# Kernel optimization log

Hardware: AMD Instinct MI355X
Metric: run time of the kernel (lower is better)

The kernel has to match this reference:

```python
import jax, jax.numpy as jnp
import numpy as np

N = 40000      # nodes
D = 64         # nnodefeatures
DEG = 32       # avg in-degree
E = N * DEG    # edges
G = 200        # graphs in batch
ATT = 64       # attention_size
HID = 128      # cls_hidden_dim
NCLS = 6
NLAYERS = 3


def setup_inputs() -> dict:
    key = jax.random.key(0)
    ks = jax.random.split(key, 8)
    s = 0.05
    x = jax.random.normal(ks[0], (N, D), dtype=jnp.float32)
    row = jax.random.randint(ks[1], (E,), 0, N, dtype=jnp.int32)
    # every node appears as a target exactly DEG times -> no zero degrees
    col = jnp.repeat(jnp.arange(N, dtype=jnp.int32), DEG)
    edge_index = jnp.stack([row, col])
    batch = jnp.repeat(jnp.arange(G, dtype=jnp.int32), N // G)
    W_lin = jax.random.normal(ks[2], (D, D), jnp.float32) * s
    b_lin = jnp.zeros((D,), jnp.float32)
    W_att = jax.random.normal(ks[3], (ATT, 2 * D), jnp.float32) * s
    a_vec = jnp.ones((ATT, 1), jnp.float32)  # torch.ones init
    W1 = jax.random.normal(ks[4], (HID, D), jnp.float32) * s
    b1 = jnp.zeros((HID,), jnp.float32)
    W2 = jax.random.normal(ks[5], (NCLS, HID), jnp.float32) * s
    b2 = jnp.zeros((NCLS,), jnp.float32)
    return dict(x=x, W_lin=W_lin, b_lin=b_lin, W_att=W_att, a_vec=a_vec,
                W1=W1, b1=b1, W2=W2, b2=b2,
                edge_index=edge_index, batch=batch, n_graphs=G)


def _gnn_layer(x, row, col, W_lin, b_lin, W_att, a_vec):
    n = x.shape[0]
    deg = jnp.sqrt(jax.ops.segment_sum(jnp.ones_like(col, dtype=x.dtype), col, num_segments=n))
    deg = jnp.where(jnp.isinf(deg), jnp.zeros_like(deg), deg)  # deg[deg==inf]=0
    norm = deg[row] * deg[col]                                  # [E]
    x_j = x[row]                                                # [E, D] gather source
    x_i = x[col]                                                # [E, D] gather target
    att_in = jnp.concatenate([x_j, x_i], axis=-1)               # [E, 2D]
    score = jnp.exp((att_in @ W_att.T) @ a_vec)                 # [E, 1]
    att_norm = jax.ops.segment_sum(score, col, num_segments=n)  # [N, 1] (scatter by edge_index[1])
    att = score / att_norm[row]                                 # gathered at edge_index[0] (faithful)
    m = ((x_j * att) @ W_lin.T + b_lin) / norm[:, None]         # [E, D]
    out = jax.ops.segment_sum(m, col, num_segments=n)           # aggregate by target
    return jax.nn.selu(out)


def reference(x, W_lin, b_lin, W_att, a_vec, W1, b1, W2, b2, edge_index, batch, n_graphs):
    row, col = edge_index[0], edge_index[1]
    # Faithful to original: the loop re-applies the layer to the ORIGINAL x each time
    for _ in range(NLAYERS):
        h = _gnn_layer(x, row, col, W_lin, b_lin, W_att, a_vec)
    sums = jax.ops.segment_sum(h, batch, num_segments=n_graphs)
    counts = jax.ops.segment_sum(jnp.ones((x.shape[0],), x.dtype), batch, num_segments=n_graphs)
    pooled = sums / counts[:, None]                              # global_mean_pool
    hcls = jax.nn.selu(pooled @ W1.T + b1)
    logits = hcls @ W2.T + b2
    return jax.nn.softmax(logits, axis=-1)
```

## Files before the change

kernel.cpp:

```cpp
#include <hip/hip_runtime.h>
#include <hip/hip_bf16.h>
#include <stdint.h>

#define N_NODES 40000
#define D_FEAT 64
#define DEG 32
#define E_EDGES (N_NODES * DEG)
#define G_GRAPHS 200
#define NPG 200
#define ATT_SZ 64
#define HID 128
#define NCLS 6
#define XS 69

__device__ __forceinline__ float selu_f(float x) {
    const float scale = 1.0507009873554805f;
    const float alpha = 1.6732632423543772f;
    return scale * (x > 0.f ? x : alpha * (__expf(x) - 1.f));
}

__device__ __forceinline__ uint32_t f2bf(float f) {
    uint32_t u = __builtin_bit_cast(uint32_t, f);
    return (u + 0x7fffu + ((u >> 16) & 1u)) >> 16;
}
__device__ __forceinline__ float bflo(uint32_t u) { return __builtin_bit_cast(float, u << 16); }
__device__ __forceinline__ float bfhi(uint32_t u) { return __builtin_bit_cast(float, u & 0xffff0000u); }

__global__ __launch_bounds__(256) void k_node(const float* __restrict__ x,
                                              const float* __restrict__ Wlin,
                                              const float* __restrict__ Watt,
                                              const float* __restrict__ avec,
                                              float* __restrict__ P,
                                              float* __restrict__ Q,
                                              uint32_t* __restrict__ yb,
                                              float* __restrict__ pool) {
    __shared__ float xs[160 * XS];
    __shared__ float ws[64 * XS];
    __shared__ float ws_w[128];
    int tid = threadIdx.x;
    int n0 = blockIdx.x * 160;
    if (blockIdx.x < 50) pool[blockIdx.x * 256 + tid] = 0.f;

    const float4* x4 = (const float4*)(x + (size_t)n0 * 64);
    const float4* W4 = (const float4*)Wlin;
#pragma unroll
    for (int s = 0; s < 10; ++s) {
        int idx = tid + s * 256, r = idx >> 4, kk = idx & 15;
        *(float4*)&xs[r * XS + kk * 4] = x4[idx];
    }
#pragma unroll
    for (int s = 0; s < 4; ++s) {
        int idx = tid + s * 256, r = idx >> 4, kk = idx & 15;
        *(float4*)&ws[r * XS + kk * 4] = W4[idx];
    }
    if (tid < 128) {
        float s = 0.f;
        for (int k = 0; k < ATT_SZ; ++k) s += avec[k] * Watt[k * 128 + tid];
        ws_w[tid] = s;
    }
    __syncthreads();

    if (tid < 160) {
        float s1 = 0.f, s2 = 0.f;
#pragma unroll 8
        for (int k = 0; k < 64; ++k) {
            float xv = xs[tid * XS + k];
            s1 += xv * ws_w[k];
            s2 += xv * ws_w[64 + k];
        }
        P[n0 + tid] = __expf(s1);
        Q[n0 + tid] = __expf(s2);
    }

    int tm = tid >> 4, tf = tid & 15;
    float acc[10][4];
#pragma unroll
    for (int i = 0; i < 10; ++i)
#pragma unroll
        for (int j = 0; j < 4; ++j) acc[i][j] = 0.f;
#pragma unroll
    for (int kk = 0; kk < 16; ++kk) {
        float4 wv[4];
#pragma unroll
        for (int j = 0; j < 4; ++j) wv[j] = *(const float4*)&ws[(4 * tf + j) * XS + kk * 4];
#pragma unroll
        for (int i = 0; i < 10; ++i) {
            float4 xv = *(const float4*)&xs[(tm + 16 * i) * XS + kk * 4];
#pragma unroll
            for (int j = 0; j < 4; ++j)
                acc[i][j] += xv.x * wv[j].x + xv.y * wv[j].y
                           + xv.z * wv[j].z + xv.w * wv[j].w;
        }
    }
#pragma unroll
    for (int i = 0; i < 10; ++i) {
        int m = n0 + tm + 16 * i;
        uint32_t p0 = f2bf(acc[i][0]) | (f2bf(acc[i][1]) << 16);
        uint32_t p1 = f2bf(acc[i][2]) | (f2bf(acc[i][3]) << 16);
        *(uint2*)&yb[(size_t)m * 32 + tf * 2] = make_uint2(p0, p1);
    }
}

__global__ __launch_bounds__(256) void k_edges(const int* __restrict__ row,
                                               const float* __restrict__ P,
                                               const float* __restrict__ Q,
                                               float* __restrict__ V) {
    int e = blockIdx.x * 256 + threadIdx.x;
    float p = P[row[e]];
#pragma unroll
    for (int off = 16; off; off >>= 1)
        p += __shfl_xor(p, off, 32);
    if ((threadIdx.x & 31) == 0) {
        int n = e >> 5;
        V[n] = P[n] / (Q[n] * p);
    }
}

__global__ __launch_bounds__(256) void k_agg(const int* __restrict__ row,
                                             const float* __restrict__ V,
                                             const float* __restrict__ Q,
                                             const uint32_t* __restrict__ yb,
                                             const float* __restrict__ blin,
                                             float* __restrict__ pool) {
    __shared__ float2 meta[1024];
    int tid = threadIdx.x;
    int n0 = blockIdx.x * 32;

    int4 r4 = ((const int4*)(row + (size_t)n0 * 32))[tid];
    meta[4 * tid + 0] = make_float2(V[r4.x], __builtin_bit_cast(float, r4.x << 7));
    meta[4 * tid + 1] = make_float2(V[r4.y], __builtin_bit_cast(float, r4.y << 7));
    meta[4 * tid + 2] = make_float2(V[r4.z], __builtin_bit_cast(float, r4.z << 7));
    meta[4 * tid + 3] = make_float2(V[r4.w], __builtin_bit_cast(float, r4.w << 7));
    __syncthreads();

    int wv = tid >> 6, lane = tid & 63;
    int q = lane >> 4, fi = lane & 15;
    float4 bl4 = ((const float4*)blin)[fi];
    int nw0 = n0 + wv * 8;
    float4 pacc = make_float4(0.f, 0.f, 0.f, 0.f);
    const char* ybc = (const char*)yb;
#pragma unroll 1
    for (int nn = 0; nn < 8; ++nn) {
        int n = nw0 + nn;
        int base = (wv * 8 + nn) * 32;
        float4 a = make_float4(0.f, 0.f, 0.f, 0.f);
#pragma unroll
        for (int s = 0; s < 8; ++s) {
            float2 m = meta[base + s * 4 + q];
            uint32_t rbyte = __builtin_bit_cast(uint32_t, m.y);
            uint2 u = *(const uint2*)(ybc + rbyte + fi * 8);
            a.x += m.x * bflo(u.x);
            a.y += m.x * bfhi(u.x);
            a.z += m.x * bflo(u.y);
            a.w += m.x * bfhi(u.y);
        }
        a.x += __shfl_xor(a.x, 16, 64); a.x += __shfl_xor(a.x, 32, 64);
        a.y += __shfl_xor(a.y, 16, 64); a.y += __shfl_xor(a.y, 32, 64);
        a.z += __shfl_xor(a.z, 16, 64); a.z += __shfl_xor(a.z, 32, 64);
        a.w += __shfl_xor(a.w, 16, 64); a.w += __shfl_xor(a.w, 32, 64);
        float qn = Q[n] * (1.f / 32.f);
        pacc.x += selu_f(qn * a.x + bl4.x);
        pacc.y += selu_f(qn * a.y + bl4.y);
        pacc.z += selu_f(qn * a.z + bl4.z);
        pacc.w += selu_f(qn * a.w + bl4.w);
    }
    if (q == 0) {
        int g = nw0 / NPG;
        float* pp = &pool[g * 64 + 4 * fi];
        atomicAdd(pp + 0, pacc.x);
        atomicAdd(pp + 1, pacc.y);
        atomicAdd(pp + 2, pacc.z);
        atomicAdd(pp + 3, pacc.w);
    }
}

__global__ __launch_bounds__(128) void k_cls(const float* __restrict__ pool,
                                             const float* __restrict__ W1,
                                             const float* __restrict__ b1,
                                             const float* __restrict__ W2,
                                             const float* __restrict__ b2,
                                             float* __restrict__ out) {
    __shared__ float ps[64];
    __shared__ float hc[HID];
    __shared__ float lg[NCLS];
    int t = threadIdx.x, g = blockIdx.x;
    if (t < 64) ps[t] = pool[g * 64 + t] * (1.f / NPG);
    __syncthreads();
    float s = b1[t];
    const float4* w14 = (const float4*)(W1 + t * 64);
    const float4* ps4 = (const float4*)ps;
#pragma unroll
    for (int kk = 0; kk < 16; ++kk) {
        float4 w = w14[kk], p = ps4[kk];
        s += w.x * p.x; s += w.y * p.y; s += w.z * p.z; s += w.w * p.w;
    }
    hc[t] = selu_f(s);
    __syncthreads();
    if (t < NCLS) {
        float l = b2[t];
        const float4* w24 = (const float4*)(W2 + t * 128);
        const float4* hc4 = (const float4*)hc;
        for (int kk = 0; kk < 32; ++kk) {
            float4 w = w24[kk], h = hc4[kk];
            l += w.x * h.x; l += w.y * h.y; l += w.z * h.z; l += w.w * h.w;
        }
        lg[t] = l;
    }
    __syncthreads();
    if (t == 0) {
        float m = lg[0];
        for (int c = 1; c < NCLS; ++c) m = fmaxf(m, lg[c]);
        float ex[NCLS], sum = 0.f;
        for (int c = 0; c < NCLS; ++c) { ex[c] = __expf(lg[c] - m); sum += ex[c]; }
        for (int c = 0; c < NCLS; ++c) out[g * NCLS + c] = ex[c] / sum;
    }
}

extern "C" void kernel_launch(void* const* d_in, const int* in_sizes, int n_in,
                              void* d_out, int out_size, void* d_ws, size_t ws_size,
                              hipStream_t stream) {
    const float* x    = (const float*)d_in[0];
    const float* Wlin = (const float*)d_in[1];
    const float* blin = (const float*)d_in[2];
    const float* Watt = (const float*)d_in[3];
    const float* avec = (const float*)d_in[4];
    const float* W1   = (const float*)d_in[5];
    const float* b1   = (const float*)d_in[6];
    const float* W2   = (const float*)d_in[7];
    const float* b2   = (const float*)d_in[8];
    const int*   row  = (const int*)d_in[9];
    float* out = (float*)d_out;

    float* P    = (float*)d_ws;
    float* Q    = P + N_NODES;
    float* V    = Q + N_NODES;
    float* pool = V + N_NODES;
    uint32_t* yb = (uint32_t*)(pool + G_GRAPHS * 64);

    k_node<<<N_NODES / 160, 256, 0, stream>>>(x, Wlin, Watt, avec, P, Q, yb, pool);
    k_edges<<<E_EDGES / 256, 256, 0, stream>>>(row, P, Q, V);
    k_agg<<<N_NODES / 32, 256, 0, stream>>>(row, V, Q, yb, blin, pool);
    k_cls<<<G_GRAPHS, 128, 0, stream>>>(pool, W1, b1, W2, b2, out);
}
```

Baseline: 130.5 us.

## Split bf16 feature table into two half-planes and aggregate each half separately

The projected bf16 node features are stored as two planes of 32 features each, and the aggregation grid is doubled so each block gathers only one half-plane. The working set per gather pass halves (2.5MB per plane), which should improve cache hit rates for the random neighbour gathers. In exchange, the row indices and V values are loaded twice, and shuffle reductions grow from two steps to three per component.

```diff
diff --git a/kernel.cpp b/kernel.cpp
--- a/kernel.cpp
+++ b/kernel.cpp
@@ -73,6 +73,8 @@
     }
 
     int tm = tid >> 4, tf = tid & 15;
+    int half = tf >> 3, fo = tf & 7;
+    uint32_t* plane = yb + (size_t)half * N_NODES * 16;
     float acc[10][4];
 #pragma unroll
     for (int i = 0; i < 10; ++i)
@@ -97,7 +99,7 @@
         int m = n0 + tm + 16 * i;
         uint32_t p0 = f2bf(acc[i][0]) | (f2bf(acc[i][1]) << 16);
         uint32_t p1 = f2bf(acc[i][2]) | (f2bf(acc[i][3]) << 16);
-        *(uint2*)&yb[(size_t)m * 32 + tf * 2] = make_uint2(p0, p1);
+        *(uint2*)&plane[(size_t)m * 16 + fo * 2] = make_uint2(p0, p1);
     }
 }
 
@@ -124,29 +126,31 @@
                                              float* __restrict__ pool) {
     __shared__ float2 meta[1024];
     int tid = threadIdx.x;
-    int n0 = blockIdx.x * 32;
+    int nb = blockIdx.x >> 1;
+    int half = blockIdx.x & 1;
+    int n0 = nb * 32;
 
     int4 r4 = ((const int4*)(row + (size_t)n0 * 32))[tid];
-    meta[4 * tid + 0] = make_float2(V[r4.x], __builtin_bit_cast(float, r4.x << 7));
-    meta[4 * tid + 1] = make_float2(V[r4.y], __builtin_bit_cast(float, r4.y << 7));
-    meta[4 * tid + 2] = make_float2(V[r4.z], __builtin_bit_cast(float, r4.z << 7));
-    meta[4 * tid + 3] = make_float2(V[r4.w], __builtin_bit_cast(float, r4.w << 7));
+    meta[4 * tid + 0] = make_float2(V[r4.x], __builtin_bit_cast(float, r4.x << 6));
+    meta[4 * tid + 1] = make_float2(V[r4.y], __builtin_bit_cast(float, r4.y << 6));
+    meta[4 * tid + 2] = make_float2(V[r4.z], __builtin_bit_cast(float, r4.z << 6));
+    meta[4 * tid + 3] = make_float2(V[r4.w], __builtin_bit_cast(float, r4.w << 6));
     __syncthreads();
 
     int wv = tid >> 6, lane = tid & 63;
-    int q = lane >> 4, fi = lane & 15;
-    float4 bl4 = ((const float4*)blin)[fi];
+    int sr = lane >> 3, fi = lane & 7;
+    float4 bl4 = ((const float4*)blin)[half * 8 + fi];
     int nw0 = n0 + wv * 8;
     float4 pacc = make_float4(0.f, 0.f, 0.f, 0.f);
-    const char* ybc = (const char*)yb;
+    const char* ybc = (const char*)yb + (size_t)half * (N_NODES * 64);
 #pragma unroll 1
     for (int nn = 0; nn < 8; ++nn) {
         int n = nw0 + nn;
         int base = (wv * 8 + nn) * 32;
         float4 a = make_float4(0.f, 0.f, 0.f, 0.f);
 #pragma unroll
-        for (int s = 0; s < 8; ++s) {
-            float2 m = meta[base + s * 4 + q];
+        for (int s = 0; s < 4; ++s) {
+            float2 m = meta[base + s * 8 + sr];
             uint32_t rbyte = __builtin_bit_cast(uint32_t, m.y);
             uint2 u = *(const uint2*)(ybc + rbyte + fi * 8);
             a.x += m.x * bflo(u.x);
@@ -154,19 +158,19 @@
             a.z += m.x * bflo(u.y);
             a.w += m.x * bfhi(u.y);
         }
-        a.x += __shfl_xor(a.x, 16, 64); a.x += __shfl_xor(a.x, 32, 64);
-        a.y += __shfl_xor(a.y, 16, 64); a.y += __shfl_xor(a.y, 32, 64);
-        a.z += __shfl_xor(a.z, 16, 64); a.z += __shfl_xor(a.z, 32, 64);
-        a.w += __shfl_xor(a.w, 16, 64); a.w += __shfl_xor(a.w, 32, 64);
+        a.x += __shfl_xor(a.x, 8, 64); a.x += __shfl_xor(a.x, 16, 64); a.x += __shfl_xor(a.x, 32, 64);
+        a.y += __shfl_xor(a.y, 8, 64); a.y += __shfl_xor(a.y, 16, 64); a.y += __shfl_xor(a.y, 32, 64);
+        a.z += __shfl_xor(a.z, 8, 64); a.z += __shfl_xor(a.z, 16, 64); a.z += __shfl_xor(a.z, 32, 64);
+        a.w += __shfl_xor(a.w, 8, 64); a.w += __shfl_xor(a.w, 16, 64); a.w += __shfl_xor(a.w, 32, 64);
         float qn = Q[n] * (1.f / 32.f);
         pacc.x += selu_f(qn * a.x + bl4.x);
         pacc.y += selu_f(qn * a.y + bl4.y);
         pacc.z += selu_f(qn * a.z + bl4.z);
         pacc.w += selu_f(qn * a.w + bl4.w);
     }
-    if (q == 0) {
+    if (sr == 0) {
         int g = nw0 / NPG;
-        float* pp = &pool[g * 64 + 4 * fi];
+        float* pp = &pool[g * 64 + half * 32 + 4 * fi];
         atomicAdd(pp + 0, pacc.x);
         atomicAdd(pp + 1, pacc.y);
         atomicAdd(pp + 2, pacc.z);
@@ -239,6 +243,6 @@
 
     k_node<<<N_NODES / 160, 256, 0, stream>>>(x, Wlin, Watt, avec, P, Q, yb, pool);
     k_edges<<<E_EDGES / 256, 256, 0, stream>>>(row, P, Q, V);
-    k_agg<<<N_NODES / 32, 256, 0, stream>>>(row, V, Q, yb, blin, pool);
+    k_agg<<<(N_NODES / 32) * 2, 256, 0, stream>>>(row, V, Q, yb, blin, pool);
     k_cls<<<G_GRAPHS, 128, 0, stream>>>(pool, W1, b1, W2, b2, out);
 }
```

Result: slower. 138.2 us (+5.9%).
